# Optimization experiments

Hardware: AMD Instinct MI355X
Metric: run time of the kernel (lower is better)

The kernel has to match this reference:

```python
import jax, jax.numpy as jnp
import numpy as np

N_EMBD = 1024
HEAD_SIZE = 64
B, T = 4, 4096


def setup_inputs() -> dict:
    key = jax.random.key(0)
    kx, kq, kk, kv = jax.random.split(key, 4)
    x = jax.random.normal(kx, (B, T, N_EMBD), dtype=jnp.float32)
    Wq = jax.random.normal(kq, (N_EMBD, HEAD_SIZE), dtype=jnp.float32) * (N_EMBD ** -0.5)
    Wk = jax.random.normal(kk, (N_EMBD, HEAD_SIZE), dtype=jnp.float32) * (N_EMBD ** -0.5)
    Wv = jax.random.normal(kv, (N_EMBD, HEAD_SIZE), dtype=jnp.float32) * (N_EMBD ** -0.5)
    return {"x": x, "Wq": Wq, "Wk": Wk, "Wv": Wv}


def reference(x, Wq, Wk, Wv):
    # x: [B, T, C]; projections: [B, T, H]
    Bv, Tv, C = x.shape
    q = jnp.einsum('btc,ch->bth', x, Wq)
    k = jnp.einsum('btc,ch->bth', x, Wk)
    v = jnp.einsum('btc,ch->bth', x, Wv)
    # NOTE: original scales by C**-0.5 where C = n_embd (not head_size)
    scale = C ** -0.5
    wei = jnp.einsum('bth,bsh->bts', q, k) * scale  # [B, T, T]
    causal = jnp.tril(jnp.ones((Tv, Tv), dtype=bool))
    wei = jnp.where(causal[None, :, :], wei, -jnp.inf)
    wei = jax.nn.softmax(wei, axis=-1)
    # dropout p=0.0 (eval) -> identity
    out = jnp.einsum('bts,bsh->bth', wei, v)  # [B, T, H]
    return out
```

## Files before the change

### kernel.cpp

```cpp
#include <hip/hip_runtime.h>
#include <math.h>

#define Tt 4096
#define Cc 1024
#define Hh 64

typedef __attribute__((ext_vector_type(8))) short bf16x8;
typedef __attribute__((ext_vector_type(4))) float f32x4;
typedef unsigned int u32;

__device__ inline unsigned short f2bf(float f) {
    unsigned u = __float_as_uint(f);
    u = (u + 0x7FFFu + ((u >> 16) & 1u)) >> 16;
    return (unsigned short)u;
}

__global__ __launch_bounds__(256) void wt_build(
    const float* __restrict__ Wq, const float* __restrict__ Wk,
    const float* __restrict__ Wv, unsigned short* __restrict__ Wt)
{
    int e = blockIdx.x * 256 + threadIdx.x;
    int k = e & 1023, n = e >> 10;
    float v;
    if (n < 64)       v = Wq[k * 64 + n] * 0.03125f;
    else if (n < 128) v = Wk[k * 64 + (n - 64)];
    else              v = Wv[k * 64 + (n - 128)];
    Wt[n * 1024 + k] = f2bf(v);
}

__global__ __launch_bounds__(256, 2) void qkv_gemm(
    const float* __restrict__ x, const unsigned short* __restrict__ wt,
    unsigned short* __restrict__ qb, unsigned short* __restrict__ kb,
    unsigned short* __restrict__ vt)
{
    __shared__ unsigned short as_[32 * 1024];

    const int t = threadIdx.x, w = t >> 6, lane = t & 63;
    const int col = lane & 15, quad = lane >> 4;
    const int m0 = blockIdx.x * 32;

    {
        const float* xb = x + (long)m0 * Cc;
        float4 vbuf[16];
#pragma unroll
        for (int g = 0; g < 2; ++g) {
#pragma unroll
            for (int s = 0; s < 16; ++s) {
                int row = g * 16 + s;
                vbuf[s] = *(const float4*)&xb[row * 1024 + t * 4];
            }
#pragma unroll
            for (int s = 0; s < 16; ++s) {
                int row = g * 16 + s;
                ushort4 pk = { f2bf(vbuf[s].x), f2bf(vbuf[s].y),
                               f2bf(vbuf[s].z), f2bf(vbuf[s].w) };
                int woff = (t * 4) ^ ((row & 7) << 3);
                *(ushort4*)&as_[row * 1024 + woff] = pk;
            }
        }
    }
    __syncthreads();

    const unsigned short* aB[2];
#pragma unroll
    for (int kc = 0; kc < 2; ++kc)
        aB[kc] = &as_[col * 1024 + ((kc * 32 + quad * 8) ^ ((col & 7) << 3))];

    const unsigned short* pB[3];
#pragma unroll
    for (int nt = 0; nt < 3; ++nt)
        pB[nt] = wt + ((w * 3 + nt) * 16 + col) * 1024 + quad * 8;

    f32x4 acc[2][3];
#pragma unroll
    for (int mt = 0; mt < 2; ++mt)
#pragma unroll
        for (int nt = 0; nt < 3; ++nt) acc[mt][nt] = (f32x4){0.f, 0.f, 0.f, 0.f};

    bf16x8 bfr[2][3][2];
    bf16x8 afr[2][2][2];

#pragma unroll
    for (int nt = 0; nt < 3; ++nt)
#pragma unroll
        for (int kc = 0; kc < 2; ++kc)
            bfr[0][nt][kc] = *(const bf16x8*)(pB[nt] + kc * 32);
#pragma unroll
    for (int mt = 0; mt < 2; ++mt)
#pragma unroll
        for (int kc = 0; kc < 2; ++kc)
            afr[0][mt][kc] = *(const bf16x8*)(aB[kc] + mt * 16 * 1024);

#pragma unroll
    for (int k = 0; k < 16; ++k) {
        const int cur = k & 1, nxt = cur ^ 1;
        if (k < 15) {
            const int ko = (k + 1) * 64;
#pragma unroll
            for (int nt = 0; nt < 3; ++nt)
#pragma unroll
                for (int kc = 0; kc < 2; ++kc)
                    bfr[nxt][nt][kc] = *(const bf16x8*)(pB[nt] + ko + kc * 32);
#pragma unroll
            for (int mt = 0; mt < 2; ++mt)
#pragma unroll
                for (int kc = 0; kc < 2; ++kc)
                    afr[nxt][mt][kc] = *(const bf16x8*)(aB[kc] + mt * 16 * 1024 + ko);
        }
#pragma unroll
        for (int kc = 0; kc < 2; ++kc)
#pragma unroll
            for (int nt = 0; nt < 3; ++nt)
#pragma unroll
                for (int mt = 0; mt < 2; ++mt)
                    acc[mt][nt] = __builtin_amdgcn_mfma_f32_16x16x32_bf16(
                        afr[cur][mt][kc], bfr[cur][nt][kc], acc[mt][nt], 0, 0, 0);
    }

    const long bidx = m0 >> 12;
    const int tbase = m0 & 4095;
#pragma unroll
    for (int mt = 0; mt < 2; ++mt)
#pragma unroll
        for (int nt = 0; nt < 3; ++nt) {
            int ntg = w * 3 + nt;
            int n = ntg * 16 + col;
            int row = m0 + mt * 16 + quad * 4;
            if (ntg < 4) {
#pragma unroll
                for (int reg = 0; reg < 4; ++reg)
                    qb[(long)(row + reg) * Hh + n] = f2bf(acc[mt][nt][reg]);
            } else if (ntg < 8) {
#pragma unroll
                for (int reg = 0; reg < 4; ++reg)
                    kb[(long)(row + reg) * Hh + (n - 64)] = f2bf(acc[mt][nt][reg]);
            } else {
                int h = n - 128;
                ushort4 pk = { f2bf(acc[mt][nt][0]), f2bf(acc[mt][nt][1]),
                               f2bf(acc[mt][nt][2]), f2bf(acc[mt][nt][3]) };
                *(ushort4*)&vt[(bidx * Hh + h) * (long)Tt + tbase + mt * 16 + quad * 4] = pk;
            }
        }
}

#define LDP 56
#define LDO 68

__global__ __launch_bounds__(256) void attn(
    const unsigned short* __restrict__ qg, const unsigned short* __restrict__ kg,
    const unsigned short* __restrict__ vtg,
    float* __restrict__ po, float* __restrict__ pls)
{
    __shared__ __align__(16) char smem[35328];
    float* o_red       = (float*)smem;
    float* lred        = (float*)(smem + 34816);
    unsigned short* pl = (unsigned short*)smem;

    const int p    = blockIdx.x;
    const int qt   = 127 - (p >> 3);
    const int b    = p & 3;
    const int half = (p >> 2) & 1;
    const int tid  = (b << 7) | qt;
    const long qrow0 = (long)b * Tt + qt * 32;
    const int nkt = qt + 1;
    const int n0  = (nkt + 1) >> 1;
    const int cnt = half ? (nkt - n0) : n0;
    const int ust = half ? n0 : 0;

    const int t = threadIdx.x, w = t >> 6, lane = t & 63;
    const int col = lane & 15, quad = lane >> 4;
    const int plbase = w * 4352;

    bf16x8 qf[2][2];
#pragma unroll
    for (int mt = 0; mt < 2; ++mt)
#pragma unroll
        for (int kc = 0; kc < 2; ++kc)
            qf[mt][kc] = *(const bf16x8*)&qg[(qrow0 + mt * 16 + col) * Hh + kc * 32 + quad * 8];

    f32x4 oacc[2][4];
#pragma unroll
    for (int mt = 0; mt < 2; ++mt)
#pragma unroll
        for (int nt = 0; nt < 4; ++nt) oacc[mt][nt] = (f32x4){0.f, 0.f, 0.f, 0.f};
    float lsum[2][4] = {{0.f,0.f,0.f,0.f},{0.f,0.f,0.f,0.f}};

    for (int iu = w; iu < cnt; iu += 4) {
        const int u = ust + iu;
        const long krow0 = (long)b * Tt + u * 32;
        bf16x8 kf[2][2];
#pragma unroll
        for (int nt = 0; nt < 2; ++nt)
#pragma unroll
            for (int kc = 0; kc < 2; ++kc)
                kf[nt][kc] = *(const bf16x8*)&kg[(krow0 + nt * 16 + col) * Hh + kc * 32 + quad * 8];
        f32x4 s[2][2];
#pragma unroll
        for (int mt = 0; mt < 2; ++mt)
#pragma unroll
            for (int nt = 0; nt < 2; ++nt) {
                s[mt][nt] = (f32x4){0.f, 0.f, 0.f, 0.f};
#pragma unroll
                for (int kc = 0; kc < 2; ++kc)
                    s[mt][nt] = __builtin_amdgcn_mfma_f32_16x16x32_bf16(qf[mt][kc], kf[nt][kc], s[mt][nt], 0, 0, 0);
            }
#pragma unroll
        for (int mt = 0; mt < 2; ++mt)
#pragma unroll
            for (int reg = 0; reg < 4; ++reg) {
                int rloc = mt * 16 + quad * 4 + reg;
                if (u == qt) {
                    if (col > rloc)      s[mt][0][reg] = -INFINITY;
                    if (16 + col > rloc) s[mt][1][reg] = -INFINITY;
                }
                float p0 = __expf(s[mt][0][reg]);
                float p1 = __expf(s[mt][1][reg]);
                lsum[mt][reg] += p0 + p1;
                pl[plbase + rloc * LDP + col]      = f2bf(p0);
                pl[plbase + rloc * LDP + 16 + col] = f2bf(p1);
            }
        bf16x8 af0 = *(const bf16x8*)&pl[plbase + col * LDP + quad * 8];
        bf16x8 af1 = *(const bf16x8*)&pl[plbase + (16 + col) * LDP + quad * 8];
#pragma unroll
        for (int nt = 0; nt < 4; ++nt) {
            bf16x8 vf = *(const bf16x8*)&vtg[((long)b * Hh + nt * 16 + col) * Tt + u * 32 + quad * 8];
            oacc[0][nt] = __builtin_amdgcn_mfma_f32_16x16x32_bf16(af0, vf, oacc[0][nt], 0, 0, 0);
            oacc[1][nt] = __builtin_amdgcn_mfma_f32_16x16x32_bf16(af1, vf, oacc[1][nt], 0, 0, 0);
        }
    }

#pragma unroll
    for (int mt = 0; mt < 2; ++mt)
#pragma unroll
        for (int reg = 0; reg < 4; ++reg) {
            float l = lsum[mt][reg];
            l += __shfl_xor(l, 1); l += __shfl_xor(l, 2);
            l += __shfl_xor(l, 4); l += __shfl_xor(l, 8);
            if (col == 0) lred[w * 32 + mt * 16 + quad * 4 + reg] = l;
        }
#pragma unroll
    for (int mt = 0; mt < 2; ++mt)
#pragma unroll
        for (int nt = 0; nt < 4; ++nt)
#pragma unroll
            for (int reg = 0; reg < 4; ++reg)
                o_red[(w * 32 + mt * 16 + quad * 4 + reg) * LDO + nt * 16 + col] = oacc[mt][nt][reg];
    __syncthreads();
    if (t < 32)
        pls[(tid * 2 + half) * 32 + t] = lred[t] + lred[32 + t] + lred[64 + t] + lred[96 + t];
    float* pob = po + ((long)tid * 2 + half) * 2048;
#pragma unroll
    for (int j = 0; j < 8; ++j) {
        int e = t + 256 * j, r = e >> 6, c = e & 63;
        pob[e] = o_red[r * LDO + c] + o_red[(32 + r) * LDO + c]
               + o_red[(64 + r) * LDO + c] + o_red[(96 + r) * LDO + c];
    }
}

__global__ __launch_bounds__(256) void combine(
    const float* __restrict__ po, const float* __restrict__ pls, float* __restrict__ out)
{
    const int g = blockIdx.x;
    const long orow = (((long)(g >> 7)) * Tt + (long)(g & 127) * 32) * Hh;
    const float* p0 = po + (long)g * 2 * 2048;
    const float* p1 = p0 + 2048;
    const float* l0 = pls + g * 2 * 32;
    const float* l1 = l0 + 32;
    const int t = threadIdx.x;
#pragma unroll
    for (int j = 0; j < 8; ++j) {
        int e = t + 256 * j, r = e >> 6;
        out[orow + e] = (p0[e] + p1[e]) / (l0[r] + l1[r]);
    }
}

extern "C" void kernel_launch(void* const* d_in, const int* in_sizes, int n_in,
                              void* d_out, int out_size, void* d_ws, size_t ws_size,
                              hipStream_t stream)
{
    const float* x  = (const float*)d_in[0];
    const float* Wq = (const float*)d_in[1];
    const float* Wk = (const float*)d_in[2];
    const float* Wv = (const float*)d_in[3];
    float* outp = (float*)d_out;

    unsigned short* wt = (unsigned short*)d_ws;
    unsigned short* qb = wt + 196608;
    unsigned short* kb = qb + 1048576;
    unsigned short* vt = kb + 1048576;
    float* po  = (float*)(vt + 1048576);
    float* pls = po + 2097152;

    wt_build<<<dim3(768), dim3(256), 0, stream>>>(Wq, Wk, Wv, wt);
    qkv_gemm<<<dim3(512), dim3(256), 0, stream>>>(x, wt, qb, kb, vt);
    attn<<<dim3(1024), dim3(256), 0, stream>>>(qb, kb, vt, po, pls);
    combine<<<dim3(512), dim3(256), 0, stream>>>(po, pls, outp);
}
```

Measured before the change: 160.0 us.

## Store weights, Q, K, V in MFMA-fragment-native layout for coalesced loads

Writes the packed weight matrix and the Q, K and V^T intermediates in an order that matches the MFMA operand fragments. Each lane's bf16x8 load is then a contiguous 16-byte slice of a 1KB block, so every wave load is fully coalesced instead of strided across rows. The cost is scattered 2-byte stores in the GEMM epilogue and in the weight build, plus more complex index arithmetic there.

```diff
diff --git a/kernel.cpp b/kernel.cpp
--- a/kernel.cpp
+++ b/kernel.cpp
@@ -20,12 +20,19 @@
     const float* __restrict__ Wv, unsigned short* __restrict__ Wt)
 {
     int e = blockIdx.x * 256 + threadIdx.x;
-    int k = e & 1023, n = e >> 10;
+    int j    = e & 7;
+    int lane = (e >> 3) & 63;
+    int kc   = (e >> 9) & 1;
+    int ks   = (e >> 10) & 15;
+    int ntg  = e >> 14;
+    int col = lane & 15, quad = lane >> 4;
+    int n = ntg * 16 + col;
+    int k = ks * 64 + kc * 32 + quad * 8 + j;
     float v;
     if (n < 64)       v = Wq[k * 64 + n] * 0.03125f;
     else if (n < 128) v = Wk[k * 64 + (n - 64)];
     else              v = Wv[k * 64 + (n - 128)];
-    Wt[n * 1024 + k] = f2bf(v);
+    Wt[e] = f2bf(v);
 }
 
 __global__ __launch_bounds__(256, 2) void qkv_gemm(
@@ -69,7 +76,7 @@
     const unsigned short* pB[3];
 #pragma unroll
     for (int nt = 0; nt < 3; ++nt)
-        pB[nt] = wt + ((w * 3 + nt) * 16 + col) * 1024 + quad * 8;
+        pB[nt] = wt + (w * 3 + nt) * 16384 + lane * 8;
 
     f32x4 acc[2][3];
 #pragma unroll
@@ -84,7 +91,7 @@
     for (int nt = 0; nt < 3; ++nt)
 #pragma unroll
         for (int kc = 0; kc < 2; ++kc)
-            bfr[0][nt][kc] = *(const bf16x8*)(pB[nt] + kc * 32);
+            bfr[0][nt][kc] = *(const bf16x8*)(pB[nt] + kc * 512);
 #pragma unroll
     for (int mt = 0; mt < 2; ++mt)
 #pragma unroll
@@ -100,7 +107,7 @@
             for (int nt = 0; nt < 3; ++nt)
 #pragma unroll
                 for (int kc = 0; kc < 2; ++kc)
-                    bfr[nxt][nt][kc] = *(const bf16x8*)(pB[nt] + ko + kc * 32);
+                    bfr[nxt][nt][kc] = *(const bf16x8*)(pB[nt] + (k + 1) * 1024 + kc * 512);
 #pragma unroll
             for (int mt = 0; mt < 2; ++mt)
 #pragma unroll
@@ -117,28 +124,39 @@
                         afr[cur][mt][kc], bfr[cur][nt][kc], acc[mt][nt], 0, 0, 0);
     }
 
-    const long bidx = m0 >> 12;
-    const int tbase = m0 & 4095;
+    const int tile = m0 >> 5;
 #pragma unroll
     for (int mt = 0; mt < 2; ++mt)
 #pragma unroll
         for (int nt = 0; nt < 3; ++nt) {
             int ntg = w * 3 + nt;
-            int n = ntg * 16 + col;
-            int row = m0 + mt * 16 + quad * 4;
             if (ntg < 4) {
+                int kcF   = ntg >> 1;
+                int quadF = ((ntg & 1) << 1) | (col >> 3);
+                int jF    = col & 7;
+                long base = ((long)(tile * 4 + mt * 2 + kcF)) * 512
+                          + (quadF * 16 + quad * 4) * 8 + jF;
 #pragma unroll
                 for (int reg = 0; reg < 4; ++reg)
-                    qb[(long)(row + reg) * Hh + n] = f2bf(acc[mt][nt][reg]);
+                    qb[base + reg * 8] = f2bf(acc[mt][nt][reg]);
             } else if (ntg < 8) {
+                int h = (ntg - 4) * 16 + col;
+                int kcF   = h >> 5;
+                int quadF = (h >> 3) & 3;
+                int jF    = h & 7;
+                long base = ((long)(tile * 4 + mt * 2 + kcF)) * 512
+                          + (quadF * 16 + quad * 4) * 8 + jF;
 #pragma unroll
                 for (int reg = 0; reg < 4; ++reg)
-                    kb[(long)(row + reg) * Hh + (n - 64)] = f2bf(acc[mt][nt][reg]);
+                    kb[base + reg * 8] = f2bf(acc[mt][nt][reg]);
             } else {
-                int h = n - 128;
+                int ntF = ntg - 8;
+                int toff0 = mt * 16 + quad * 4;
+                long base = ((long)(tile * 4 + ntF)) * 512
+                          + ((toff0 >> 3) * 16 + col) * 8 + (toff0 & 7);
                 ushort4 pk = { f2bf(acc[mt][nt][0]), f2bf(acc[mt][nt][1]),
                                f2bf(acc[mt][nt][2]), f2bf(acc[mt][nt][3]) };
-                *(ushort4*)&vt[(bidx * Hh + h) * (long)Tt + tbase + mt * 16 + quad * 4] = pk;
+                *(ushort4*)&vt[base] = pk;
             }
         }
 }
@@ -161,7 +179,6 @@
     const int b    = p & 3;
     const int half = (p >> 2) & 1;
     const int tid  = (b << 7) | qt;
-    const long qrow0 = (long)b * Tt + qt * 32;
     const int nkt = qt + 1;
     const int n0  = (nkt + 1) >> 1;
     const int cnt = half ? (nkt - n0) : n0;
@@ -171,12 +188,16 @@
     const int col = lane & 15, quad = lane >> 4;
     const int plbase = w * 4352;
 
+    const unsigned short* qbb = qg  + ((long)(b * 128 + qt)) * 2048 + lane * 8;
+    const unsigned short* kbb = kg  + ((long)b * 128) * 2048 + lane * 8;
+    const unsigned short* vbb = vtg + ((long)b * 128) * 2048 + lane * 8;
+
     bf16x8 qf[2][2];
 #pragma unroll
     for (int mt = 0; mt < 2; ++mt)
 #pragma unroll
         for (int kc = 0; kc < 2; ++kc)
-            qf[mt][kc] = *(const bf16x8*)&qg[(qrow0 + mt * 16 + col) * Hh + kc * 32 + quad * 8];
+            qf[mt][kc] = *(const bf16x8*)(qbb + (mt * 2 + kc) * 512);
 
     f32x4 oacc[2][4];
 #pragma unroll
@@ -187,13 +208,14 @@
 
     for (int iu = w; iu < cnt; iu += 4) {
         const int u = ust + iu;
-        const long krow0 = (long)b * Tt + u * 32;
+        const unsigned short* ku = kbb + u * 2048;
+        const unsigned short* vu = vbb + u * 2048;
         bf16x8 kf[2][2];
 #pragma unroll
         for (int nt = 0; nt < 2; ++nt)
 #pragma unroll
             for (int kc = 0; kc < 2; ++kc)
-                kf[nt][kc] = *(const bf16x8*)&kg[(krow0 + nt * 16 + col) * Hh + kc * 32 + quad * 8];
+                kf[nt][kc] = *(const bf16x8*)(ku + (nt * 2 + kc) * 512);
         f32x4 s[2][2];
 #pragma unroll
         for (int mt = 0; mt < 2; ++mt)
@@ -223,7 +245,7 @@
         bf16x8 af1 = *(const bf16x8*)&pl[plbase + (16 + col) * LDP + quad * 8];
 #pragma unroll
         for (int nt = 0; nt < 4; ++nt) {
-            bf16x8 vf = *(const bf16x8*)&vtg[((long)b * Hh + nt * 16 + col) * Tt + u * 32 + quad * 8];
+            bf16x8 vf = *(const bf16x8*)(vu + nt * 512);
             oacc[0][nt] = __builtin_amdgcn_mfma_f32_16x16x32_bf16(af0, vf, oacc[0][nt], 0, 0, 0);
             oacc[1][nt] = __builtin_amdgcn_mfma_f32_16x16x32_bf16(af1, vf, oacc[1][nt], 0, 0, 0);
         }
```

Measured after the change: 131.1 us. 18.1% less time.
